# Kernel tuning notes

Measured on AMD Instinct MI355X. Metric: run time of the kernel, lower is better.

Reference implementation:

```python
import jax, jax.numpy as jnp
import numpy as np

N_NODES = 5000
N_EDGES = 160000
HID = 64
NODE_F = 4
TASK_F = 4
BATCH = 512


def _glorot(key, shape):
    fan_in = shape[-1]
    return jax.random.normal(key, shape, dtype=jnp.float32) / jnp.sqrt(jnp.float32(fan_in))


def setup_inputs() -> dict:
    key = jax.random.key(0)
    ks = jax.random.split(key, 16)
    x = jax.random.normal(ks[0], (N_NODES, NODE_F), dtype=jnp.float32)
    edge_index = jax.random.randint(ks[1], (2, N_EDGES), 0, N_NODES, dtype=jnp.int64)
    task_feat = jax.random.normal(ks[2], (BATCH, TASK_F), dtype=jnp.float32)
    return {
        "x": x,
        "edge_index": edge_index,
        "task_feat": task_feat,
        # SAGEConv layer 1: out = lin_l(mean_neigh) + lin_r(x); lin_l has bias, lin_r (root) has no bias (PyG default)
        "Wl1": _glorot(ks[3], (HID, NODE_F)), "bl1": jnp.zeros((HID,), jnp.float32),
        "Wr1": _glorot(ks[4], (HID, NODE_F)),
        # SAGEConv layer 2
        "Wl2": _glorot(ks[5], (HID, HID)), "bl2": jnp.zeros((HID,), jnp.float32),
        "Wr2": _glorot(ks[6], (HID, HID)),
        # task_encoder: Linear(4,64) -> ReLU -> Linear(64,64)
        "Wt1": _glorot(ks[7], (HID, TASK_F)), "bt1": jnp.zeros((HID,), jnp.float32),
        "Wt2": _glorot(ks[8], (HID, HID)), "bt2": jnp.zeros((HID,), jnp.float32),
        # classifier: Linear(128,64) -> ReLU -> Linear(64,1)
        "Wc1": _glorot(ks[9], (HID, 2 * HID)), "bc1": jnp.zeros((HID,), jnp.float32),
        "Wc2": _glorot(ks[10], (1, HID)), "bc2": jnp.zeros((1,), jnp.float32),
    }


def _sage_conv(x, src, dst, Wl, bl, Wr):
    # PyG SAGEConv(mean): messages flow src -> dst; mean over incoming neighbors
    msg_sum = jax.ops.segment_sum(x[src], dst, num_segments=N_NODES)
    deg = jax.ops.segment_sum(jnp.ones((src.shape[0],), x.dtype), dst, num_segments=N_NODES)
    mean_neigh = msg_sum / jnp.maximum(deg, 1.0)[:, None]
    return mean_neigh @ Wl.T + bl + x @ Wr.T


def reference(x, edge_index, task_feat,
              Wl1, bl1, Wr1, Wl2, bl2, Wr2,
              Wt1, bt1, Wt2, bt2, Wc1, bc1, Wc2, bc2):
    src, dst = edge_index[0], edge_index[1]
    h = jax.nn.relu(_sage_conv(x, src, dst, Wl1, bl1, Wr1))        # [N, HID]
    h = jax.nn.relu(_sage_conv(h, src, dst, Wl2, bl2, Wr2))        # [N, HID]
    t = jax.nn.relu(task_feat @ Wt1.T + bt1) @ Wt2.T + bt2         # [B, HID]
    # classifier on concat([h, t]) == split Wc1 into h-part and t-part; avoids materializing the concat
    h_part = h @ Wc1[:, :HID].T                                    # [N, HID]
    t_part = t @ Wc1[:, HID:].T + bc1                              # [B, HID]
    hidden = jax.nn.relu(h_part[None, :, :] + t_part[:, None, :])  # [B, N, HID]
    scores = jnp.einsum('bnh,h->bn', hidden, Wc2[0]) + bc2[0]      # [B, N]
    return scores
```

## Files before the change

kernel.cpp:

```cpp
#include <hip/hip_runtime.h>

#define N_NODES 5000
#define N_EDGES 160000
#define HID 64
#define BATCH 512
#define NSL 64
#define EPS (N_EDGES / NSL)
#define SLOTS 12
#define NROW (NSL * SLOTS)
#define CSTRIDE 96


__global__ __launch_bounds__(256) void sort_kernel(
        const int* __restrict__ ei, const float* __restrict__ task_feat,
        const float* __restrict__ Wt1, const float* __restrict__ bt1,
        const float* __restrict__ Wt2, const float* __restrict__ bt2,
        const float* __restrict__ Wc1, const float* __restrict__ bc1,
        const float* __restrict__ Wl1, const float* __restrict__ Wr1,
        const float* __restrict__ Wl2, const float* __restrict__ Wr2,
        int* __restrict__ slots, int* __restrict__ cnt, float* __restrict__ t_part,
        float* __restrict__ Wl1T, float* __restrict__ Wr1T,
        float* __restrict__ Wl2T, float* __restrict__ Wr2T,
        float* __restrict__ Wc1hT) {
    int tid = threadIdx.x;
    int blk = blockIdx.x;
    __shared__ union SM {
        int cur[N_NODES];
        struct { float s1[4][64]; float s2[4][64]; } t;
    } sm;

    if (blk < NSL) {
        int s = blk;
        for (int i = tid; i < N_NODES; i += 256) sm.cur[i] = 0;
        __syncthreads();
        int base = s * EPS;
        for (int j = tid; j < EPS; j += 256) {
            int src = ei[base + j];
            int dst = ei[N_EDGES + base + j];
            int q = atomicAdd(&sm.cur[dst], 1);
            if (q < SLOTS) slots[dst * NROW + s * SLOTS + q] = src;
        }
        __syncthreads();
        for (int n = tid; n < N_NODES; n += 256)
            cnt[s * N_NODES + n] = min(sm.cur[n], SLOTS);
    } else if (blk < NSL + 4) {
        int w = blk - NSL;
        if (w == 0) {
            for (int idx = tid; idx < 4096; idx += 256) {
                int k = idx >> 6, h = idx & 63;
                Wl2T[idx] = Wl2[h * 64 + k];
            }
        } else if (w == 1) {
            for (int idx = tid; idx < 4096; idx += 256) {
                int k = idx >> 6, h = idx & 63;
                Wr2T[idx] = Wr2[h * 64 + k];
            }
        } else if (w == 2) {
            for (int idx = tid; idx < 4096; idx += 256) {
                int k = idx >> 6, h = idx & 63;
                Wc1hT[idx] = Wc1[h * 128 + k];
            }
        } else {
            int k = tid >> 6, h = tid & 63;
            Wl1T[tid] = Wl1[h * 4 + k];
            Wr1T[tid] = Wr1[h * 4 + k];
        }
    } else {
        int grp = tid >> 6, h = tid & 63;
        int b = (blk - (NSL + 4)) * 4 + grp;
        float4 tf = ((const float4*)task_feat)[b];
        float4 w1 = ((const float4*)Wt1)[h];
        float v = bt1[h] + tf.x * w1.x + tf.y * w1.y + tf.z * w1.z + tf.w * w1.w;
        sm.t.s1[grp][h] = fmaxf(v, 0.f);
        __syncthreads();
        const float4* w2r = (const float4*)(Wt2 + h * 64);
        const float4* s1v = (const float4*)sm.t.s1[grp];
        float v2 = bt2[h];
#pragma unroll
        for (int q = 0; q < 16; q++) {
            float4 w = w2r[q]; float4 ss = s1v[q];
            v2 += ss.x * w.x + ss.y * w.y + ss.z * w.z + ss.w * w.w;
        }
        sm.t.s2[grp][h] = v2;
        __syncthreads();
        const float4* wcr = (const float4*)(Wc1 + h * 128 + 64);
        const float4* s2v = (const float4*)sm.t.s2[grp];
        float p = bc1[h];
#pragma unroll
        for (int q = 0; q < 16; q++) {
            float4 w = wcr[q]; float4 ss = s2v[q];
            p += ss.x * w.x + ss.y * w.y + ss.z * w.z + ss.w * w.w;
        }
        t_part[b * 64 + h] = p;
    }
}

__global__ __launch_bounds__(256) void layer1_kernel(
        const float* __restrict__ x, const int* __restrict__ slots,
        const int* __restrict__ cnt,
        const float* __restrict__ Wl1T, const float* __restrict__ bl1,
        const float* __restrict__ Wr1T,
        int* __restrict__ deg, int* __restrict__ compact, float* __restrict__ h1) {
    int lane = threadIdx.x & 63, grp = threadIdx.x >> 6;
    int n = blockIdx.x * 4 + grp;
    int c = cnt[lane * N_NODES + n];
    int scan = c;
#pragma unroll
    for (int off = 1; off < 64; off <<= 1) {
        int nb = __shfl_up(scan, off);
        if (lane >= off) scan += nb;
    }
    int d = __shfl(scan, 63);
    int excl = scan - c;
    const int* chunk = slots + n * NROW + lane * SLOTS;
    float4 xs = make_float4(0.f, 0.f, 0.f, 0.f);
    for (int q = 0; q < c; q++) {
        int src = chunk[q];
        float4 xv = ((const float4*)x)[src];
        xs.x += xv.x; xs.y += xv.y; xs.z += xv.z; xs.w += xv.w;
        int pos = excl + q;
        if (pos < CSTRIDE) compact[n * CSTRIDE + pos] = src;
    }
#pragma unroll
    for (int off = 1; off < 64; off <<= 1) {
        xs.x += __shfl_xor(xs.x, off);
        xs.y += __shfl_xor(xs.y, off);
        xs.z += __shfl_xor(xs.z, off);
        xs.w += __shfl_xor(xs.w, off);
    }
    if (d > CSTRIDE) d = CSTRIDE;
    if (lane == 0) deg[n] = d;
    float inv = 1.f / fmaxf((float)d, 1.f);
    float m0 = xs.x * inv, m1 = xs.y * inv, m2 = xs.z * inv, m3 = xs.w * inv;
    float4 xn = ((const float4*)x)[n];
    float v = bl1[lane]
            + m0 * Wl1T[lane] + m1 * Wl1T[64 + lane]
            + m2 * Wl1T[128 + lane] + m3 * Wl1T[192 + lane]
            + xn.x * Wr1T[lane] + xn.y * Wr1T[64 + lane]
            + xn.z * Wr1T[128 + lane] + xn.w * Wr1T[192 + lane];
    h1[n * 64 + lane] = fmaxf(v, 0.f);
}

__global__ __launch_bounds__(256) void layer2_kernel(
        const float* __restrict__ h1, const int* __restrict__ deg,
        const int* __restrict__ compact,
        const float* __restrict__ Wl2T, const float* __restrict__ bl2,
        const float* __restrict__ Wr2T, const float* __restrict__ Wc1hT,
        float* __restrict__ h_part) {
    int h = threadIdx.x & 63, grp = threadIdx.x >> 6;
    int n = blockIdx.x * 4 + grp;
    int d = deg[n];
    const int* bucket = compact + n * CSTRIDE;
    float a0 = 0.f, a1 = 0.f, a2 = 0.f, a3 = 0.f;
    int j = 0;
    for (; j + 4 <= d; j += 4) {
        int e0 = bucket[j], e1 = bucket[j + 1], e2 = bucket[j + 2], e3 = bucket[j + 3];
        a0 += h1[e0 * 64 + h];
        a1 += h1[e1 * 64 + h];
        a2 += h1[e2 * 64 + h];
        a3 += h1[e3 * 64 + h];
    }
    for (; j < d; j++) a0 += h1[bucket[j] * 64 + h];
    float m = (a0 + a1 + a2 + a3) / fmaxf((float)d, 1.f);

    __shared__ float shm[4][64], shh[4][64], shh2[4][64];
    shm[grp][h] = m;
    shh[grp][h] = h1[n * 64 + h];
    __syncthreads();
    float v = bl2[h];
#pragma unroll
    for (int k = 0; k < 64; k++)
        v += shm[grp][k] * Wl2T[k * 64 + h] + shh[grp][k] * Wr2T[k * 64 + h];
    shh2[grp][h] = fmaxf(v, 0.f);
    __syncthreads();
    float p = 0.f;
#pragma unroll
    for (int k = 0; k < 64; k++) p += shh2[grp][k] * Wc1hT[k * 64 + h];
    h_part[n * 64 + h] = p;
}

__global__ __launch_bounds__(256) void scores_kernel(
        const float* __restrict__ h_part, const float* __restrict__ t_part,
        const float* __restrict__ Wc2, const float* __restrict__ bc2,
        float* __restrict__ out) {
    int tid = threadIdx.x;
    int n = blockIdx.x * 256 + tid;
    bool valid = n < N_NODES;
    int nn = valid ? n : (N_NODES - 1);
    float hr[64];
    const float4* hp = (const float4*)(h_part + nn * 64);
#pragma unroll
    for (int i = 0; i < 16; i++) {
        float4 v = hp[i];
        hr[4 * i + 0] = v.x; hr[4 * i + 1] = v.y;
        hr[4 * i + 2] = v.z; hr[4 * i + 3] = v.w;
    }
    float b2 = bc2[0];
    int b0 = blockIdx.y * 8;
    for (int bb = 0; bb < 8; bb++) {
        const float* tp = t_part + (b0 + bb) * 64;
        float acc = 0.f;
#pragma unroll
        for (int h = 0; h < 64; h++)
            acc = fmaf(fmaxf(hr[h] + tp[h], 0.f), Wc2[h], acc);
        if (valid) out[(b0 + bb) * N_NODES + n] = acc + b2;
    }
}

extern "C" void kernel_launch(void* const* d_in, const int* in_sizes, int n_in,
                              void* d_out, int out_size, void* d_ws, size_t ws_size,
                              hipStream_t stream) {
    const float* x    = (const float*)d_in[0];
    const int*   ei   = (const int*)d_in[1];
    const float* task = (const float*)d_in[2];
    const float* Wl1  = (const float*)d_in[3];
    const float* bl1  = (const float*)d_in[4];
    const float* Wr1  = (const float*)d_in[5];
    const float* Wl2  = (const float*)d_in[6];
    const float* bl2  = (const float*)d_in[7];
    const float* Wr2  = (const float*)d_in[8];
    const float* Wt1  = (const float*)d_in[9];
    const float* bt1  = (const float*)d_in[10];
    const float* Wt2  = (const float*)d_in[11];
    const float* bt2  = (const float*)d_in[12];
    const float* Wc1  = (const float*)d_in[13];
    const float* bc1  = (const float*)d_in[14];
    const float* Wc2  = (const float*)d_in[15];
    const float* bc2  = (const float*)d_in[16];
    float* out = (float*)d_out;

    char* ws = (char*)d_ws;
    int*   slots   = (int*)(ws + 0);
    int*   cnt     = (int*)(ws + 15360000);
    int*   compact = (int*)(ws + 16640000);
    int*   deg     = (int*)(ws + 18560000);
    float* h1      = (float*)(ws + 18580000);
    float* h_part  = (float*)(ws + 19860000);
    float* t_part  = (float*)(ws + 21140000);
    float* Wl1T  = (float*)(ws + 21271072);
    float* Wr1T  = (float*)(ws + 21272096);
    float* Wl2T  = (float*)(ws + 21273120);
    float* Wr2T  = (float*)(ws + 21289504);
    float* Wc1hT = (float*)(ws + 21305888);

    sort_kernel<<<NSL + 4 + BATCH / 4, 256, 0, stream>>>(
        ei, task, Wt1, bt1, Wt2, bt2, Wc1, bc1, Wl1, Wr1, Wl2, Wr2,
        slots, cnt, t_part, Wl1T, Wr1T, Wl2T, Wr2T, Wc1hT);
    layer1_kernel<<<N_NODES / 4, 256, 0, stream>>>(x, slots, cnt, Wl1T, bl1, Wr1T,
                                                   deg, compact, h1);
    layer2_kernel<<<N_NODES / 4, 256, 0, stream>>>(h1, deg, compact, Wl2T, bl2, Wr2T,
                                                   Wc1hT, h_part);
    scores_kernel<<<dim3(20, 64), 256, 0, stream>>>(h_part, t_part, Wc2, bc2, out);
}
```

Measured before the change: 148.1 us.

## Accumulate layer-1 neighbor feature sums during edge bucketing via LDS atomics

The edge-bucketing kernel now also sums x[src] per destination node in shared memory with float atomics, splitting the node range into two halves so the counters and float4 sums fit in LDS. Per-slice partial sums go to a new xpart buffer. Layer 1 then reads and reduces these partials instead of gathering x for every edge. This removes the dependent gather loop from layer 1, but the sort kernel reads the edge list twice and does extra LDS atomics. Float atomic order also makes summation order nondeterministic, and edges beyond the slot cap are now counted in the sum but not in the degree.

```diff
diff --git a/kernel.cpp b/kernel.cpp
--- a/kernel.cpp
+++ b/kernel.cpp
@@ -9,40 +9,60 @@
 #define SLOTS 12
 #define NROW (NSL * SLOTS)
 #define CSTRIDE 96
+#define HALF (N_NODES / 2)
 
 
 __global__ __launch_bounds__(256) void sort_kernel(
-        const int* __restrict__ ei, const float* __restrict__ task_feat,
+        const int* __restrict__ ei, const float* __restrict__ x,
+        const float* __restrict__ task_feat,
         const float* __restrict__ Wt1, const float* __restrict__ bt1,
         const float* __restrict__ Wt2, const float* __restrict__ bt2,
         const float* __restrict__ Wc1, const float* __restrict__ bc1,
         const float* __restrict__ Wl1, const float* __restrict__ Wr1,
         const float* __restrict__ Wl2, const float* __restrict__ Wr2,
-        int* __restrict__ slots, int* __restrict__ cnt, float* __restrict__ t_part,
+        int* __restrict__ slots, int* __restrict__ cnt, float4* __restrict__ xpart,
+        float* __restrict__ t_part,
         float* __restrict__ Wl1T, float* __restrict__ Wr1T,
         float* __restrict__ Wl2T, float* __restrict__ Wr2T,
         float* __restrict__ Wc1hT) {
     int tid = threadIdx.x;
     int blk = blockIdx.x;
     __shared__ union SM {
-        int cur[N_NODES];
+        struct { int cur[HALF]; float4 xs[HALF]; } a;
         struct { float s1[4][64]; float s2[4][64]; } t;
     } sm;
 
     if (blk < NSL) {
         int s = blk;
-        for (int i = tid; i < N_NODES; i += 256) sm.cur[i] = 0;
-        __syncthreads();
         int base = s * EPS;
-        for (int j = tid; j < EPS; j += 256) {
-            int src = ei[base + j];
-            int dst = ei[N_EDGES + base + j];
-            int q = atomicAdd(&sm.cur[dst], 1);
-            if (q < SLOTS) slots[dst * NROW + s * SLOTS + q] = src;
-        }
-        __syncthreads();
-        for (int n = tid; n < N_NODES; n += 256)
-            cnt[s * N_NODES + n] = min(sm.cur[n], SLOTS);
+        for (int half = 0; half < 2; half++) {
+            int n0 = half * HALF;
+            for (int i = tid; i < HALF; i += 256) {
+                sm.a.cur[i] = 0;
+                sm.a.xs[i] = make_float4(0.f, 0.f, 0.f, 0.f);
+            }
+            __syncthreads();
+            for (int j = tid; j < EPS; j += 256) {
+                int src = ei[base + j];
+                int dst = ei[N_EDGES + base + j];
+                unsigned r = (unsigned)(dst - n0);
+                if (r < (unsigned)HALF) {
+                    int q = atomicAdd(&sm.a.cur[r], 1);
+                    if (q < SLOTS) slots[dst * NROW + s * SLOTS + q] = src;
+                    float4 xv = ((const float4*)x)[src];
+                    atomicAdd(&sm.a.xs[r].x, xv.x);
+                    atomicAdd(&sm.a.xs[r].y, xv.y);
+                    atomicAdd(&sm.a.xs[r].z, xv.z);
+                    atomicAdd(&sm.a.xs[r].w, xv.w);
+                }
+            }
+            __syncthreads();
+            for (int i = tid; i < HALF; i += 256) {
+                cnt[s * N_NODES + n0 + i] = min(sm.a.cur[i], SLOTS);
+                xpart[s * N_NODES + n0 + i] = sm.a.xs[i];
+            }
+            __syncthreads();
+        }
     } else if (blk < NSL + 4) {
         int w = blk - NSL;
         if (w == 0) {
@@ -97,7 +117,7 @@
 
 __global__ __launch_bounds__(256) void layer1_kernel(
         const float* __restrict__ x, const int* __restrict__ slots,
-        const int* __restrict__ cnt,
+        const int* __restrict__ cnt, const float4* __restrict__ xpart,
         const float* __restrict__ Wl1T, const float* __restrict__ bl1,
         const float* __restrict__ Wr1T,
         int* __restrict__ deg, int* __restrict__ compact, float* __restrict__ h1) {
@@ -113,14 +133,11 @@
     int d = __shfl(scan, 63);
     int excl = scan - c;
     const int* chunk = slots + n * NROW + lane * SLOTS;
-    float4 xs = make_float4(0.f, 0.f, 0.f, 0.f);
     for (int q = 0; q < c; q++) {
-        int src = chunk[q];
-        float4 xv = ((const float4*)x)[src];
-        xs.x += xv.x; xs.y += xv.y; xs.z += xv.z; xs.w += xv.w;
         int pos = excl + q;
-        if (pos < CSTRIDE) compact[n * CSTRIDE + pos] = src;
-    }
+        if (pos < CSTRIDE) compact[n * CSTRIDE + pos] = chunk[q];
+    }
+    float4 xs = xpart[lane * N_NODES + n];
 #pragma unroll
     for (int off = 1; off < 64; off <<= 1) {
         xs.x += __shfl_xor(xs.x, off);
@@ -230,23 +247,24 @@
     float* out = (float*)d_out;
 
     char* ws = (char*)d_ws;
-    int*   slots   = (int*)(ws + 0);
-    int*   cnt     = (int*)(ws + 15360000);
-    int*   compact = (int*)(ws + 16640000);
-    int*   deg     = (int*)(ws + 18560000);
-    float* h1      = (float*)(ws + 18580000);
-    float* h_part  = (float*)(ws + 19860000);
-    float* t_part  = (float*)(ws + 21140000);
-    float* Wl1T  = (float*)(ws + 21271072);
-    float* Wr1T  = (float*)(ws + 21272096);
-    float* Wl2T  = (float*)(ws + 21273120);
-    float* Wr2T  = (float*)(ws + 21289504);
-    float* Wc1hT = (float*)(ws + 21305888);
+    int*    slots   = (int*)(ws + 0);
+    int*    cnt     = (int*)(ws + 15360000);
+    float4* xpart   = (float4*)(ws + 16640000);
+    int*    compact = (int*)(ws + 21760000);
+    int*    deg     = (int*)(ws + 23680000);
+    float*  h1      = (float*)(ws + 23700000);
+    float*  h_part  = (float*)(ws + 24980000);
+    float*  t_part  = (float*)(ws + 26260000);
+    float* Wl1T  = (float*)(ws + 26391072);
+    float* Wr1T  = (float*)(ws + 26392096);
+    float* Wl2T  = (float*)(ws + 26393120);
+    float* Wr2T  = (float*)(ws + 26409504);
+    float* Wc1hT = (float*)(ws + 26425888);
 
     sort_kernel<<<NSL + 4 + BATCH / 4, 256, 0, stream>>>(
-        ei, task, Wt1, bt1, Wt2, bt2, Wc1, bc1, Wl1, Wr1, Wl2, Wr2,
-        slots, cnt, t_part, Wl1T, Wr1T, Wl2T, Wr2T, Wc1hT);
-    layer1_kernel<<<N_NODES / 4, 256, 0, stream>>>(x, slots, cnt, Wl1T, bl1, Wr1T,
+        ei, x, task, Wt1, bt1, Wt2, bt2, Wc1, bc1, Wl1, Wr1, Wl2, Wr2,
+        slots, cnt, xpart, t_part, Wl1T, Wr1T, Wl2T, Wr2T, Wc1hT);
+    layer1_kernel<<<N_NODES / 4, 256, 0, stream>>>(x, slots, cnt, xpart, Wl1T, bl1, Wr1T,
                                                    deg, compact, h1);
     layer2_kernel<<<N_NODES / 4, 256, 0, stream>>>(h1, deg, compact, Wl2T, bl2, Wr2T,
                                                    Wc1hT, h_part);
```

After: 159.5 us. 7.7% more time.
